# Kernel optimization log

Hardware: AMD Instinct MI355X
Metric: run time of the kernel (lower is better)

## Reference

```python
import jax, jax.numpy as jnp
import numpy as np

N_VOX = 150000
GRID = 256
C_IN = 32
C_OUT = 64
EPS = 1e-5


def _build_neighbor_idx(n=N_VOX, g=GRID, seed=0):
    # Build a submanifold-conv rulebook: for each of 27 kernel offsets and each
    # output voxel, the index of the input voxel at that offset, or -1 if absent.
    rng = np.random.default_rng(seed)
    lin = rng.choice(g ** 3, size=n, replace=False).astype(np.int64)
    coords = np.stack(np.unravel_index(lin, (g, g, g)), axis=1)  # [N,3]
    order = np.argsort(lin)
    sorted_keys = lin[order]
    offs = np.array([[dx, dy, dz] for dx in (-1, 0, 1) for dy in (-1, 0, 1) for dz in (-1, 0, 1)], dtype=np.int64)  # [27,3]
    nbr = np.full((27, n), -1, dtype=np.int32)
    for k in range(27):
        nc = coords + offs[k]  # neighbor coords [N,3]
        valid = np.all((nc >= 0) & (nc < g), axis=1)
        nkey = (nc[:, 0] * g + nc[:, 1]) * g + nc[:, 2]
        pos = np.searchsorted(sorted_keys, nkey)
        pos_c = np.clip(pos, 0, n - 1)
        found = valid & (sorted_keys[pos_c] == nkey)
        nbr[k] = np.where(found, order[pos_c].astype(np.int32), -1)
    return jnp.asarray(nbr)


def setup_inputs() -> dict:
    key = jax.random.key(0)
    k1, k2, k3, k4 = jax.random.split(key, 4)
    features = jax.random.normal(k1, (N_VOX, C_IN), dtype=jnp.float32)
    weight = jax.random.normal(k2, (27, C_IN, C_OUT), dtype=jnp.float32) * 0.05
    gamma = jax.random.uniform(k3, (C_OUT,), dtype=jnp.float32, minval=0.5, maxval=1.5)
    beta = jax.random.normal(k4, (C_OUT,), dtype=jnp.float32) * 0.1
    neighbor_idx = _build_neighbor_idx()
    return {"features": features, "weight": weight, "gamma": gamma, "beta": beta, "neighbor_idx": neighbor_idx}


def reference(features, weight, gamma, beta, neighbor_idx):
    # --- SubMConv3d via rulebook gather -> GEMM -> (implicit) scatter ---
    safe_idx = jnp.maximum(neighbor_idx, 0)            # [K,N]
    gathered = features[safe_idx]                      # [K,N,Cin]
    mask = (neighbor_idx >= 0)[..., None]              # [K,N,1]
    gathered = jnp.where(mask, gathered, jnp.zeros((), features.dtype))
    out = jnp.einsum('knc,kcd->nd', gathered, weight)  # [N,Cout]
    # --- BatchNorm1d (training-mode batch stats, biased var) + ReLU ---
    mean = jnp.mean(out, axis=0)
    var = jnp.mean(jnp.square(out - mean), axis=0)
    normed = (out - mean) * jax.lax.rsqrt(var + EPS)
    return jax.nn.relu(normed * gamma + beta)
```

## Files before the change

kernel.cpp:

```cpp
#include <hip/hip_runtime.h>

#define NV    150000
#define CIN   32
#define COUT  64
#define EPSF  1e-5f
#define NCOPY 16

#define NTHR   256
#define NTILES (NV / 16)
#define NBLK1  ((NTILES + 3) / 4)

#define CH8    (NV * COUT / 8)
#define NBLK2  1172
#define STRIDE2 (NBLK2 * NTHR)

#define WS_WFRAG  0
#define WS_GSTATS 110592
#define WS_OUTBF  118784

typedef short  bf16x8 __attribute__((ext_vector_type(8)));
typedef float  f32x4  __attribute__((ext_vector_type(4)));

union u4bf { uint4 u; bf16x8 h; };

__device__ __forceinline__ unsigned pack_bf2(float a, float b) {
    union { float f; unsigned u; } ca, cb;
    ca.f = a; cb.f = b;
    const unsigned lo = (ca.u + 0x7FFFu + ((ca.u >> 16) & 1u)) >> 16;
    const unsigned hi = (cb.u + 0x7FFFu + ((cb.u >> 16) & 1u)) & 0xFFFF0000u;
    return lo | hi;
}

__device__ __forceinline__ unsigned short bf16r(float a) {
    union { float f; unsigned u; } c; c.f = a;
    return (unsigned short)((c.u + 0x7FFFu + ((c.u >> 16) & 1u)) >> 16);
}

__device__ __forceinline__ u4bf pack_row(float4 f0, float4 f1) {
    u4bf r;
    r.u.x = pack_bf2(f0.x, f0.y);
    r.u.y = pack_bf2(f0.z, f0.w);
    r.u.z = pack_bf2(f1.x, f1.y);
    r.u.w = pack_bf2(f1.z, f1.w);
    return r;
}

__global__ __launch_bounds__(NTHR) void k_prep(
    const float* __restrict__ weight,
    char*        __restrict__ ws)
{
    const int b = blockIdx.x;
    if (b < 27) {
        const int k    = b;
        const int bb   = threadIdx.x >> 6;
        const int lane = threadIdx.x & 63;
        const int quad = lane >> 4;
        const int lm   = lane & 15;
        const float* wsrc = weight + (long)k * CIN * COUT + (quad * 8) * COUT + bb * 16 + lm;
        float f[8];
#pragma unroll
        for (int j = 0; j < 8; ++j) f[j] = wsrc[j * COUT];
        uint4 o;
        o.x = pack_bf2(f[0], f[1]);
        o.y = pack_bf2(f[2], f[3]);
        o.z = pack_bf2(f[4], f[5]);
        o.w = pack_bf2(f[6], f[7]);
        ((uint4*)(ws + WS_WFRAG))[(k * 4 + bb) * 64 + lane] = o;
    } else {
        float* gs = (float*)(ws + WS_GSTATS);
#pragma unroll
        for (int i = 0; i < 8; ++i) gs[threadIdx.x + i * NTHR] = 0.f;
    }
}

__global__ __launch_bounds__(NTHR) void k_conv(
    const float* __restrict__ feat,
    char*        __restrict__ ws,
    const int*   __restrict__ nbr,
    float*       __restrict__ gstats)
{
    const uint4* wf = (const uint4*)(ws + WS_WFRAG);
    unsigned short* ob = (unsigned short*)(ws + WS_OUTBF);

    const int tid  = threadIdx.x;
    const int lane = tid & 63;
    const int quad = lane >> 4;
    const int lm   = lane & 15;
    const int wid  = blockIdx.x * 4 + (tid >> 6);

    f32x4 ssum = {0.f, 0.f, 0.f, 0.f};
    f32x4 qsum = {0.f, 0.f, 0.f, 0.f};
    f32x4 acc[4] = {{0.f,0.f,0.f,0.f},{0.f,0.f,0.f,0.f},{0.f,0.f,0.f,0.f},{0.f,0.f,0.f,0.f}};

    const bool have_tile = (wid < NTILES);
    const int v0 = have_tile ? wid * 16 : 0;

    if (have_tile) {
        int sidx[7];
#pragma unroll
        for (int it = 0; it < 7; ++it) {
            const int item = lane + it * 64;
            int idx = -1;
            if (item < 416) {
                const int kp = item >> 4;
                const int k  = kp + (kp >= 13);
                idx = nbr[(long)k * NV + v0 + (item & 15)];
            }
            sidx[it] = idx;
        }

        {
            const float4* fp = (const float4*)(feat + (long)(v0 + lm) * CIN + quad * 8);
            const u4bf a0 = pack_row(fp[0], fp[1]);
#pragma unroll
            for (int b = 0; b < 4; ++b) {
                u4bf w; w.u = wf[(13 * 4 + b) * 64 + lane];
                acc[b] = __builtin_amdgcn_mfma_f32_16x16x32_bf16(a0.h, w.h, acc[b], 0, 0, 0);
            }
        }

        unsigned int kmask = 0u;
#pragma unroll
        for (int it = 0; it < 7; ++it) {
            const unsigned long long m = __ballot(sidx[it] >= 0);
            kmask |= ((m & 0xFFFFull)         ? 1u : 0u) << (it * 4 + 0);
            kmask |= (((m >> 16) & 0xFFFFull) ? 1u : 0u) << (it * 4 + 1);
            kmask |= (((m >> 32) & 0xFFFFull) ? 1u : 0u) << (it * 4 + 2);
            kmask |= ((m >> 48)               ? 1u : 0u) << (it * 4 + 3);
        }

        while (kmask) {
            const int kpA = __ffs(kmask) - 1;
            kmask &= kmask - 1u;
            int kpB = -1;
            if (kmask) { kpB = __ffs(kmask) - 1; kmask &= kmask - 1u; }
            const int kA = kpA + (kpA >= 13);
            const int kB = (kpB >= 0) ? (kpB + (kpB >= 13)) : kA;

            int rawA, rawB;
            switch (kpA >> 2) {
                case 0: rawA = sidx[0]; break; case 1: rawA = sidx[1]; break;
                case 2: rawA = sidx[2]; break; case 3: rawA = sidx[3]; break;
                case 4: rawA = sidx[4]; break; case 5: rawA = sidx[5]; break;
                default: rawA = sidx[6]; break;
            }
            const int kpB2 = (kpB >= 0) ? kpB : kpA;
            switch (kpB2 >> 2) {
                case 0: rawB = sidx[0]; break; case 1: rawB = sidx[1]; break;
                case 2: rawB = sidx[2]; break; case 3: rawB = sidx[3]; break;
                case 4: rawB = sidx[4]; break; case 5: rawB = sidx[5]; break;
                default: rawB = sidx[6]; break;
            }
            const int idxA = __shfl(rawA, ((kpA & 3) << 4) | lm);
            int idxB = __shfl(rawB, ((kpB2 & 3) << 4) | lm);
            if (kpB < 0) idxB = -1;

            const float4* fpA = (const float4*)(feat + (long)(idxA < 0 ? 0 : idxA) * CIN + quad * 8);
            const float4* fpB = (const float4*)(feat + (long)(idxB < 0 ? 0 : idxB) * CIN + quad * 8);
            u4bf aA = pack_row(fpA[0], fpA[1]);
            u4bf aB = pack_row(fpB[0], fpB[1]);
            if (idxA < 0) aA.u = make_uint4(0u, 0u, 0u, 0u);
            if (idxB < 0) aB.u = make_uint4(0u, 0u, 0u, 0u);

#pragma unroll
            for (int b = 0; b < 4; ++b) {
                u4bf wA, wB;
                wA.u = wf[(kA * 4 + b) * 64 + lane];
                wB.u = wf[(kB * 4 + b) * 64 + lane];
                acc[b] = __builtin_amdgcn_mfma_f32_16x16x32_bf16(aA.h, wA.h, acc[b], 0, 0, 0);
                acc[b] = __builtin_amdgcn_mfma_f32_16x16x32_bf16(aB.h, wB.h, acc[b], 0, 0, 0);
            }
        }

#pragma unroll
        for (int b = 0; b < 4; ++b) {
            const float r0 = acc[b][0], r1 = acc[b][1], r2 = acc[b][2], r3 = acc[b][3];
            ob[(long)(v0 + quad * 4 + 0) * COUT + b * 16 + lm] = bf16r(r0);
            ob[(long)(v0 + quad * 4 + 1) * COUT + b * 16 + lm] = bf16r(r1);
            ob[(long)(v0 + quad * 4 + 2) * COUT + b * 16 + lm] = bf16r(r2);
            ob[(long)(v0 + quad * 4 + 3) * COUT + b * 16 + lm] = bf16r(r3);
            ssum[b] += r0 + r1 + r2 + r3;
            qsum[b] += r0 * r0 + r1 * r1 + r2 * r2 + r3 * r3;
        }
    }

#pragma unroll
    for (int off = 16; off < 64; off <<= 1) {
#pragma unroll
        for (int b = 0; b < 4; ++b) {
            ssum[b] += __shfl_xor(ssum[b], off);
            qsum[b] += __shfl_xor(qsum[b], off);
        }
    }

    __shared__ float ls[4][128];
    const int wv = tid >> 6;
    if (quad == 0) {
#pragma unroll
        for (int b = 0; b < 4; ++b) {
            ls[wv][b * 16 + lm]      = ssum[b];
            ls[wv][64 + b * 16 + lm] = qsum[b];
        }
    }
    __syncthreads();
    if (tid < 128) {
        const float v = ls[0][tid] + ls[1][tid] + ls[2][tid] + ls[3][tid];
        atomicAdd(gstats + (blockIdx.x & (NCOPY - 1)) * 128 + tid, v);
    }
}

__global__ __launch_bounds__(NTHR) void k_norm(
    const char*  __restrict__ ws_ro,
    float*       __restrict__ out,
    const float* __restrict__ gstats,
    const float* __restrict__ gamma,
    const float* __restrict__ beta)
{
    __shared__ float sscale[COUT];
    __shared__ float sshift[COUT];
    const int tid = threadIdx.x;
    if (tid < COUT) {
        float s = 0.f, q = 0.f;
#pragma unroll
        for (int cp = 0; cp < NCOPY; ++cp) {
            s += gstats[cp * 128 + tid];
            q += gstats[cp * 128 + 64 + tid];
        }
        const float inv_n = 1.f / (float)NV;
        const float mean = s * inv_n;
        float var = q * inv_n - mean * mean;
        var = fmaxf(var, 0.f);
        const float rstd = rsqrtf(var + EPSF);
        const float sc = gamma[tid] * rstd;
        sscale[tid] = sc;
        sshift[tid] = beta[tid] - mean * sc;
    }
    __syncthreads();

    const int  base = blockIdx.x * NTHR + tid;
    const int  g8   = (base & 7) * 8;
    const float4 SC0 = make_float4(sscale[g8],   sscale[g8+1], sscale[g8+2], sscale[g8+3]);
    const float4 SC1 = make_float4(sscale[g8+4], sscale[g8+5], sscale[g8+6], sscale[g8+7]);
    const float4 SH0 = make_float4(sshift[g8],   sshift[g8+1], sshift[g8+2], sshift[g8+3]);
    const float4 SH1 = make_float4(sshift[g8+4], sshift[g8+5], sshift[g8+6], sshift[g8+7]);

    const uint4* ib = (const uint4*)(ws_ro + WS_OUTBF);
    float4* o4 = (float4*)out;

#pragma unroll
    for (int n = 0; n < 4; ++n) {
        const int c = base + n * STRIDE2;
        if (n == 3 && c >= CH8) break;
        const uint4 u = ib[c];
        union { unsigned u; float f; } t;
        float4 v0, v1;
        t.u = u.x << 16;          v0.x = t.f;
        t.u = u.x & 0xFFFF0000u;  v0.y = t.f;
        t.u = u.y << 16;          v0.z = t.f;
        t.u = u.y & 0xFFFF0000u;  v0.w = t.f;
        t.u = u.z << 16;          v1.x = t.f;
        t.u = u.z & 0xFFFF0000u;  v1.y = t.f;
        t.u = u.w << 16;          v1.z = t.f;
        t.u = u.w & 0xFFFF0000u;  v1.w = t.f;

        v0.x = fmaxf(v0.x * SC0.x + SH0.x, 0.f);
        v0.y = fmaxf(v0.y * SC0.y + SH0.y, 0.f);
        v0.z = fmaxf(v0.z * SC0.z + SH0.z, 0.f);
        v0.w = fmaxf(v0.w * SC0.w + SH0.w, 0.f);
        v1.x = fmaxf(v1.x * SC1.x + SH1.x, 0.f);
        v1.y = fmaxf(v1.y * SC1.y + SH1.y, 0.f);
        v1.z = fmaxf(v1.z * SC1.z + SH1.z, 0.f);
        v1.w = fmaxf(v1.w * SC1.w + SH1.w, 0.f);

        o4[(long)c * 2]     = v0;
        o4[(long)c * 2 + 1] = v1;
    }
}

extern "C" void kernel_launch(void* const* d_in, const int* in_sizes, int n_in,
                              void* d_out, int out_size, void* d_ws, size_t ws_size,
                              hipStream_t stream) {
    const float* feat   = (const float*)d_in[0];
    const float* weight = (const float*)d_in[1];
    const float* gamma  = (const float*)d_in[2];
    const float* beta   = (const float*)d_in[3];
    const int*   nbr    = (const int*)d_in[4];
    float* out = (float*)d_out;

    char*  ws     = (char*)d_ws;
    float* gstats = (float*)(ws + WS_GSTATS);

    k_prep<<<28, NTHR, 0, stream>>>(weight, ws);
    k_conv<<<NBLK1, NTHR, 0, stream>>>(feat, ws, nbr, gstats);
    k_norm<<<NBLK2, NTHR, 0, stream>>>(ws, out, gstats, gamma, beta);
}
```

Baseline: 114.7 us.

## Fuse conv and batchnorm into persistent kernel with grid barrier

Merges the conv and normalize kernels into one persistent kernel of 512 blocks, where each wave handles 5 tiles and keeps their accumulators in registers. A software grid barrier on an atomic counter waits for the global statistics before scale and shift are applied straight from registers. This removes the bf16 intermediate write and re-read and one kernel launch, and prefetches the next tile's neighbor indices. In exchange it needs all 512 blocks co-resident (launch bounds set to 2 blocks per CU), uses far more registers per wave, and its output stores are narrow scalar writes.

```diff
diff --git a/kernel.cpp b/kernel.cpp
--- a/kernel.cpp
+++ b/kernel.cpp
@@ -8,15 +8,13 @@
 
 #define NTHR   256
 #define NTILES (NV / 16)
-#define NBLK1  ((NTILES + 3) / 4)
-
-#define CH8    (NV * COUT / 8)
-#define NBLK2  1172
-#define STRIDE2 (NBLK2 * NTHR)
+#define NBLKF  512
+#define WAVES_TOT (NBLKF * 4)
+#define TPW    5
 
 #define WS_WFRAG  0
 #define WS_GSTATS 110592
-#define WS_OUTBF  118784
+#define WS_BAR    (WS_GSTATS + NCOPY * 128 * 4)
 
 typedef short  bf16x8 __attribute__((ext_vector_type(8)));
 typedef float  f32x4  __attribute__((ext_vector_type(4)));
@@ -29,11 +27,6 @@
     const unsigned lo = (ca.u + 0x7FFFu + ((ca.u >> 16) & 1u)) >> 16;
     const unsigned hi = (cb.u + 0x7FFFu + ((cb.u >> 16) & 1u)) & 0xFFFF0000u;
     return lo | hi;
-}
-
-__device__ __forceinline__ unsigned short bf16r(float a) {
-    union { float f; unsigned u; } c; c.f = a;
-    return (unsigned short)((c.u + 0x7FFFu + ((c.u >> 16) & 1u)) >> 16);
 }
 
 __device__ __forceinline__ u4bf pack_row(float4 f0, float4 f1) {
@@ -69,18 +62,37 @@
     } else {
         float* gs = (float*)(ws + WS_GSTATS);
 #pragma unroll
-        for (int i = 0; i < 8; ++i) gs[threadIdx.x + i * NTHR] = 0.f;
-    }
-}
-
-__global__ __launch_bounds__(NTHR) void k_conv(
+        for (int i = 0; i < 9; ++i) gs[threadIdx.x + i * NTHR] = 0.f;
+    }
+}
+
+__device__ __forceinline__ void load_sidx(
+    const int* __restrict__ nbr, int v0, bool have, int lane, int sidx[7])
+{
+#pragma unroll
+    for (int it = 0; it < 7; ++it) {
+        const int item = lane + it * 64;
+        int idx = -1;
+        if (have && item < 416) {
+            const int kp = item >> 4;
+            const int k  = kp + (kp >= 13);
+            idx = nbr[(long)k * NV + v0 + (item & 15)];
+        }
+        sidx[it] = idx;
+    }
+}
+
+__global__ __launch_bounds__(NTHR, 2) void k_fused(
     const float* __restrict__ feat,
     char*        __restrict__ ws,
     const int*   __restrict__ nbr,
-    float*       __restrict__ gstats)
+    float*       __restrict__ gstats,
+    float*       __restrict__ out,
+    const float* __restrict__ gamma,
+    const float* __restrict__ beta)
 {
     const uint4* wf = (const uint4*)(ws + WS_WFRAG);
-    unsigned short* ob = (unsigned short*)(ws + WS_OUTBF);
+    unsigned* bar = (unsigned*)(ws + WS_BAR);
 
     const int tid  = threadIdx.x;
     const int lane = tid & 63;
@@ -90,97 +102,103 @@
 
     f32x4 ssum = {0.f, 0.f, 0.f, 0.f};
     f32x4 qsum = {0.f, 0.f, 0.f, 0.f};
-    f32x4 acc[4] = {{0.f,0.f,0.f,0.f},{0.f,0.f,0.f,0.f},{0.f,0.f,0.f,0.f},{0.f,0.f,0.f,0.f}};
-
-    const bool have_tile = (wid < NTILES);
-    const int v0 = have_tile ? wid * 16 : 0;
-
-    if (have_tile) {
-        int sidx[7];
-#pragma unroll
-        for (int it = 0; it < 7; ++it) {
-            const int item = lane + it * 64;
-            int idx = -1;
-            if (item < 416) {
-                const int kp = item >> 4;
-                const int k  = kp + (kp >= 13);
-                idx = nbr[(long)k * NV + v0 + (item & 15)];
-            }
-            sidx[it] = idx;
-        }
-
-        {
-            const float4* fp = (const float4*)(feat + (long)(v0 + lm) * CIN + quad * 8);
-            const u4bf a0 = pack_row(fp[0], fp[1]);
+    f32x4 acc[TPW][4];
+#pragma unroll
+    for (int t = 0; t < TPW; ++t)
+#pragma unroll
+        for (int b = 0; b < 4; ++b) acc[t][b] = (f32x4){0.f, 0.f, 0.f, 0.f};
+
+    int sidx[7];
+    load_sidx(nbr, wid * 16, wid < NTILES, lane, sidx);
+
+#pragma unroll
+    for (int t = 0; t < TPW; ++t) {
+        const int tile = wid + t * WAVES_TOT;
+        const bool have = (tile < NTILES);
+        const int v0 = tile * 16;
+
+        int snxt[7];
+        if (t + 1 < TPW) {
+            const int tn = wid + (t + 1) * WAVES_TOT;
+            load_sidx(nbr, tn * 16, tn < NTILES, lane, snxt);
+        }
+
+        if (have) {
+            {
+                const float4* fp = (const float4*)(feat + (long)(v0 + lm) * CIN + quad * 8);
+                const u4bf a0 = pack_row(fp[0], fp[1]);
+#pragma unroll
+                for (int b = 0; b < 4; ++b) {
+                    u4bf w; w.u = wf[(13 * 4 + b) * 64 + lane];
+                    acc[t][b] = __builtin_amdgcn_mfma_f32_16x16x32_bf16(a0.h, w.h, acc[t][b], 0, 0, 0);
+                }
+            }
+
+            unsigned int kmask = 0u;
+#pragma unroll
+            for (int it = 0; it < 7; ++it) {
+                const unsigned long long m = __ballot(sidx[it] >= 0);
+                kmask |= ((m & 0xFFFFull)         ? 1u : 0u) << (it * 4 + 0);
+                kmask |= (((m >> 16) & 0xFFFFull) ? 1u : 0u) << (it * 4 + 1);
+                kmask |= (((m >> 32) & 0xFFFFull) ? 1u : 0u) << (it * 4 + 2);
+                kmask |= ((m >> 48)               ? 1u : 0u) << (it * 4 + 3);
+            }
+
+            while (kmask) {
+                const int kpA = __ffs(kmask) - 1;
+                kmask &= kmask - 1u;
+                int kpB = -1;
+                if (kmask) { kpB = __ffs(kmask) - 1; kmask &= kmask - 1u; }
+                const int kA = kpA + (kpA >= 13);
+                const int kB = (kpB >= 0) ? (kpB + (kpB >= 13)) : kA;
+
+                int rawA, rawB;
+                switch (kpA >> 2) {
+                    case 0: rawA = sidx[0]; break; case 1: rawA = sidx[1]; break;
+                    case 2: rawA = sidx[2]; break; case 3: rawA = sidx[3]; break;
+                    case 4: rawA = sidx[4]; break; case 5: rawA = sidx[5]; break;
+                    default: rawA = sidx[6]; break;
+                }
+                const int kpB2 = (kpB >= 0) ? kpB : kpA;
+                switch (kpB2 >> 2) {
+                    case 0: rawB = sidx[0]; break; case 1: rawB = sidx[1]; break;
+                    case 2: rawB = sidx[2]; break; case 3: rawB = sidx[3]; break;
+                    case 4: rawB = sidx[4]; break; case 5: rawB = sidx[5]; break;
+                    default: rawB = sidx[6]; break;
+                }
+                const int idxA = __shfl(rawA, ((kpA & 3) << 4) | lm);
+                int idxB = __shfl(rawB, ((kpB2 & 3) << 4) | lm);
+                if (kpB < 0) idxB = -1;
+
+                const float4* fpA = (const float4*)(feat + (long)(idxA < 0 ? 0 : idxA) * CIN + quad * 8);
+                const float4* fpB = (const float4*)(feat + (long)(idxB < 0 ? 0 : idxB) * CIN + quad * 8);
+                u4bf aA = pack_row(fpA[0], fpA[1]);
+                u4bf aB = pack_row(fpB[0], fpB[1]);
+                if (idxA < 0) aA.u = make_uint4(0u, 0u, 0u, 0u);
+                if (idxB < 0) aB.u = make_uint4(0u, 0u, 0u, 0u);
+
+#pragma unroll
+                for (int b = 0; b < 4; ++b) {
+                    u4bf wA, wB;
+                    wA.u = wf[(kA * 4 + b) * 64 + lane];
+                    wB.u = wf[(kB * 4 + b) * 64 + lane];
+                    acc[t][b] = __builtin_amdgcn_mfma_f32_16x16x32_bf16(aA.h, wA.h, acc[t][b], 0, 0, 0);
+                    acc[t][b] = __builtin_amdgcn_mfma_f32_16x16x32_bf16(aB.h, wB.h, acc[t][b], 0, 0, 0);
+                }
+            }
+
 #pragma unroll
             for (int b = 0; b < 4; ++b) {
-                u4bf w; w.u = wf[(13 * 4 + b) * 64 + lane];
-                acc[b] = __builtin_amdgcn_mfma_f32_16x16x32_bf16(a0.h, w.h, acc[b], 0, 0, 0);
-            }
-        }
-
-        unsigned int kmask = 0u;
-#pragma unroll
-        for (int it = 0; it < 7; ++it) {
-            const unsigned long long m = __ballot(sidx[it] >= 0);
-            kmask |= ((m & 0xFFFFull)         ? 1u : 0u) << (it * 4 + 0);
-            kmask |= (((m >> 16) & 0xFFFFull) ? 1u : 0u) << (it * 4 + 1);
-            kmask |= (((m >> 32) & 0xFFFFull) ? 1u : 0u) << (it * 4 + 2);
-            kmask |= ((m >> 48)               ? 1u : 0u) << (it * 4 + 3);
-        }
-
-        while (kmask) {
-            const int kpA = __ffs(kmask) - 1;
-            kmask &= kmask - 1u;
-            int kpB = -1;
-            if (kmask) { kpB = __ffs(kmask) - 1; kmask &= kmask - 1u; }
-            const int kA = kpA + (kpA >= 13);
-            const int kB = (kpB >= 0) ? (kpB + (kpB >= 13)) : kA;
-
-            int rawA, rawB;
-            switch (kpA >> 2) {
-                case 0: rawA = sidx[0]; break; case 1: rawA = sidx[1]; break;
-                case 2: rawA = sidx[2]; break; case 3: rawA = sidx[3]; break;
-                case 4: rawA = sidx[4]; break; case 5: rawA = sidx[5]; break;
-                default: rawA = sidx[6]; break;
-            }
-            const int kpB2 = (kpB >= 0) ? kpB : kpA;
-            switch (kpB2 >> 2) {
-                case 0: rawB = sidx[0]; break; case 1: rawB = sidx[1]; break;
-                case 2: rawB = sidx[2]; break; case 3: rawB = sidx[3]; break;
-                case 4: rawB = sidx[4]; break; case 5: rawB = sidx[5]; break;
-                default: rawB = sidx[6]; break;
-            }
-            const int idxA = __shfl(rawA, ((kpA & 3) << 4) | lm);
-            int idxB = __shfl(rawB, ((kpB2 & 3) << 4) | lm);
-            if (kpB < 0) idxB = -1;
-
-            const float4* fpA = (const float4*)(feat + (long)(idxA < 0 ? 0 : idxA) * CIN + quad * 8);
-            const float4* fpB = (const float4*)(feat + (long)(idxB < 0 ? 0 : idxB) * CIN + quad * 8);
-            u4bf aA = pack_row(fpA[0], fpA[1]);
-            u4bf aB = pack_row(fpB[0], fpB[1]);
-            if (idxA < 0) aA.u = make_uint4(0u, 0u, 0u, 0u);
-            if (idxB < 0) aB.u = make_uint4(0u, 0u, 0u, 0u);
-
-#pragma unroll
-            for (int b = 0; b < 4; ++b) {
-                u4bf wA, wB;
-                wA.u = wf[(kA * 4 + b) * 64 + lane];
-                wB.u = wf[(kB * 4 + b) * 64 + lane];
-                acc[b] = __builtin_amdgcn_mfma_f32_16x16x32_bf16(aA.h, wA.h, acc[b], 0, 0, 0);
-                acc[b] = __builtin_amdgcn_mfma_f32_16x16x32_bf16(aB.h, wB.h, acc[b], 0, 0, 0);
-            }
-        }
-
-#pragma unroll
-        for (int b = 0; b < 4; ++b) {
-            const float r0 = acc[b][0], r1 = acc[b][1], r2 = acc[b][2], r3 = acc[b][3];
-            ob[(long)(v0 + quad * 4 + 0) * COUT + b * 16 + lm] = bf16r(r0);
-            ob[(long)(v0 + quad * 4 + 1) * COUT + b * 16 + lm] = bf16r(r1);
-            ob[(long)(v0 + quad * 4 + 2) * COUT + b * 16 + lm] = bf16r(r2);
-            ob[(long)(v0 + quad * 4 + 3) * COUT + b * 16 + lm] = bf16r(r3);
-            ssum[b] += r0 + r1 + r2 + r3;
-            qsum[b] += r0 * r0 + r1 * r1 + r2 * r2 + r3 * r3;
+                const float r0 = acc[t][b][0], r1 = acc[t][b][1];
+                const float r2 = acc[t][b][2], r3 = acc[t][b][3];
+                ssum[b] += r0 + r1 + r2 + r3;
+                qsum[b] += r0 * r0 + r1 * r1 + r2 * r2 + r3 * r3;
+            }
+        }
+
+        if (t + 1 < TPW) {
+#pragma unroll
+            for (int it = 0; it < 7; ++it) sidx[it] = snxt[it];
         }
     }
 
@@ -207,24 +225,25 @@
         const float v = ls[0][tid] + ls[1][tid] + ls[2][tid] + ls[3][tid];
         atomicAdd(gstats + (blockIdx.x & (NCOPY - 1)) * 128 + tid, v);
     }
-}
-
-__global__ __launch_bounds__(NTHR) void k_norm(
-    const char*  __restrict__ ws_ro,
-    float*       __restrict__ out,
-    const float* __restrict__ gstats,
-    const float* __restrict__ gamma,
-    const float* __restrict__ beta)
-{
+    __syncthreads();
+
+    if (tid == 0) {
+        __threadfence();
+        __hip_atomic_fetch_add(bar, 1u, __ATOMIC_ACQ_REL, __HIP_MEMORY_SCOPE_AGENT);
+        while (__hip_atomic_load(bar, __ATOMIC_ACQUIRE, __HIP_MEMORY_SCOPE_AGENT) < (unsigned)NBLKF) {
+            __builtin_amdgcn_s_sleep(8);
+        }
+    }
+    __syncthreads();
+
     __shared__ float sscale[COUT];
     __shared__ float sshift[COUT];
-    const int tid = threadIdx.x;
     if (tid < COUT) {
         float s = 0.f, q = 0.f;
 #pragma unroll
         for (int cp = 0; cp < NCOPY; ++cp) {
-            s += gstats[cp * 128 + tid];
-            q += gstats[cp * 128 + 64 + tid];
+            s += __hip_atomic_load(gstats + cp * 128 + tid, __ATOMIC_RELAXED, __HIP_MEMORY_SCOPE_AGENT);
+            q += __hip_atomic_load(gstats + cp * 128 + 64 + tid, __ATOMIC_RELAXED, __HIP_MEMORY_SCOPE_AGENT);
         }
         const float inv_n = 1.f / (float)NV;
         const float mean = s * inv_n;
@@ -237,43 +256,26 @@
     }
     __syncthreads();
 
-    const int  base = blockIdx.x * NTHR + tid;
-    const int  g8   = (base & 7) * 8;
-    const float4 SC0 = make_float4(sscale[g8],   sscale[g8+1], sscale[g8+2], sscale[g8+3]);
-    const float4 SC1 = make_float4(sscale[g8+4], sscale[g8+5], sscale[g8+6], sscale[g8+7]);
-    const float4 SH0 = make_float4(sshift[g8],   sshift[g8+1], sshift[g8+2], sshift[g8+3]);
-    const float4 SH1 = make_float4(sshift[g8+4], sshift[g8+5], sshift[g8+6], sshift[g8+7]);
-
-    const uint4* ib = (const uint4*)(ws_ro + WS_OUTBF);
-    float4* o4 = (float4*)out;
-
-#pragma unroll
-    for (int n = 0; n < 4; ++n) {
-        const int c = base + n * STRIDE2;
-        if (n == 3 && c >= CH8) break;
-        const uint4 u = ib[c];
-        union { unsigned u; float f; } t;
-        float4 v0, v1;
-        t.u = u.x << 16;          v0.x = t.f;
-        t.u = u.x & 0xFFFF0000u;  v0.y = t.f;
-        t.u = u.y << 16;          v0.z = t.f;
-        t.u = u.y & 0xFFFF0000u;  v0.w = t.f;
-        t.u = u.z << 16;          v1.x = t.f;
-        t.u = u.z & 0xFFFF0000u;  v1.y = t.f;
-        t.u = u.w << 16;          v1.z = t.f;
-        t.u = u.w & 0xFFFF0000u;  v1.w = t.f;
-
-        v0.x = fmaxf(v0.x * SC0.x + SH0.x, 0.f);
-        v0.y = fmaxf(v0.y * SC0.y + SH0.y, 0.f);
-        v0.z = fmaxf(v0.z * SC0.z + SH0.z, 0.f);
-        v0.w = fmaxf(v0.w * SC0.w + SH0.w, 0.f);
-        v1.x = fmaxf(v1.x * SC1.x + SH1.x, 0.f);
-        v1.y = fmaxf(v1.y * SC1.y + SH1.y, 0.f);
-        v1.z = fmaxf(v1.z * SC1.z + SH1.z, 0.f);
-        v1.w = fmaxf(v1.w * SC1.w + SH1.w, 0.f);
-
-        o4[(long)c * 2]     = v0;
-        o4[(long)c * 2 + 1] = v1;
+    float scv[4], shv[4];
+#pragma unroll
+    for (int b = 0; b < 4; ++b) {
+        scv[b] = sscale[b * 16 + lm];
+        shv[b] = sshift[b * 16 + lm];
+    }
+
+#pragma unroll
+    for (int t = 0; t < TPW; ++t) {
+        const int tile = wid + t * WAVES_TOT;
+        if (tile >= NTILES) continue;
+        const int v0 = tile * 16;
+#pragma unroll
+        for (int b = 0; b < 4; ++b) {
+#pragma unroll
+            for (int r = 0; r < 4; ++r) {
+                out[(long)(v0 + quad * 4 + r) * COUT + b * 16 + lm] =
+                    fmaxf(acc[t][b][r] * scv[b] + shv[b], 0.f);
+            }
+        }
     }
 }
 
@@ -291,6 +293,5 @@
     float* gstats = (float*)(ws + WS_GSTATS);
 
     k_prep<<<28, NTHR, 0, stream>>>(weight, ws);
-    k_conv<<<NBLK1, NTHR, 0, stream>>>(feat, ws, nbr, gstats);
-    k_norm<<<NBLK2, NTHR, 0, stream>>>(ws, out, gstats, gamma, beta);
-}
+    k_fused<<<NBLKF, NTHR, 0, stream>>>(feat, ws, nbr, gstats, out, gamma, beta);
+}
```

New measurement: 210.6 us. +83.6%, slower.

## Split conv into dense center-offset MFMA pass and sparse atomic scatter pass

Applied to the files above, without the earlier changes.

Replaces the per-tile rulebook conv with two kernels. A dense kernel computes only the center offset with bf16 MFMA and writes an fp32 intermediate. A sparse kernel then walks each of the other 26 offsets, does an fp32 dot product for each valid neighbor, and scatters it with atomicAdd. Batch statistics are updated incrementally from the value returned by each atomic, so the squared-sum terms telescope to the final total. The aim is to avoid per-tile index gathering and MFMA work on the very sparse neighbor sets, at the cost of an extra launch, atomic traffic, and an fp32 intermediate buffer twice the size of the previous bf16 one.

```diff
diff --git a/kernel.cpp b/kernel.cpp
--- a/kernel.cpp
+++ b/kernel.cpp
@@ -5,18 +5,19 @@
 #define COUT  64
 #define EPSF  1e-5f
 #define NCOPY 16
-
-#define NTHR   256
-#define NTILES (NV / 16)
-#define NBLK1  ((NTILES + 3) / 4)
-
-#define CH8    (NV * COUT / 8)
-#define NBLK2  1172
-#define STRIDE2 (NBLK2 * NTHR)
-
-#define WS_WFRAG  0
-#define WS_GSTATS 110592
-#define WS_OUTBF  118784
+#define NTHR  256
+
+#define NTILES 9375
+#define NBLKD  2344
+#define VBLK   586
+#define NBLK3  1172
+#define STRIDE3 (NBLK3 * NTHR)
+#define CH4    (NV * COUT / 4)
+
+#define WS_WT     0
+#define WS_W13    221184
+#define WS_GSTATS 225280
+#define WS_OUTF   233472
 
 typedef short  bf16x8 __attribute__((ext_vector_type(8)));
 typedef float  f32x4  __attribute__((ext_vector_type(4)));
@@ -29,11 +30,6 @@
     const unsigned lo = (ca.u + 0x7FFFu + ((ca.u >> 16) & 1u)) >> 16;
     const unsigned hi = (cb.u + 0x7FFFu + ((cb.u >> 16) & 1u)) & 0xFFFF0000u;
     return lo | hi;
-}
-
-__device__ __forceinline__ unsigned short bf16r(float a) {
-    union { float f; unsigned u; } c; c.f = a;
-    return (unsigned short)((c.u + 0x7FFFu + ((c.u >> 16) & 1u)) >> 16);
 }
 
 __device__ __forceinline__ u4bf pack_row(float4 f0, float4 f1) {
@@ -51,12 +47,22 @@
 {
     const int b = blockIdx.x;
     if (b < 27) {
-        const int k    = b;
+        const int k = b;
+        float* wt = (float*)(ws + WS_WT) + (long)k * COUT * CIN;
+        const float* wsrc = weight + (long)k * CIN * COUT;
+#pragma unroll
+        for (int e = 0; e < 8; ++e) {
+            const int idx = threadIdx.x + e * NTHR;
+            const int ci  = idx >> 6;
+            const int co  = idx & 63;
+            wt[co * CIN + ci] = wsrc[ci * COUT + co];
+        }
+    } else if (b == 27) {
         const int bb   = threadIdx.x >> 6;
         const int lane = threadIdx.x & 63;
         const int quad = lane >> 4;
         const int lm   = lane & 15;
-        const float* wsrc = weight + (long)k * CIN * COUT + (quad * 8) * COUT + bb * 16 + lm;
+        const float* wsrc = weight + (long)13 * CIN * COUT + (quad * 8) * COUT + bb * 16 + lm;
         float f[8];
 #pragma unroll
         for (int j = 0; j < 8; ++j) f[j] = wsrc[j * COUT];
@@ -65,7 +71,7 @@
         o.y = pack_bf2(f[2], f[3]);
         o.z = pack_bf2(f[4], f[5]);
         o.w = pack_bf2(f[6], f[7]);
-        ((uint4*)(ws + WS_WFRAG))[(k * 4 + bb) * 64 + lane] = o;
+        ((uint4*)(ws + WS_W13))[bb * 64 + lane] = o;
     } else {
         float* gs = (float*)(ws + WS_GSTATS);
 #pragma unroll
@@ -73,112 +79,41 @@
     }
 }
 
-__global__ __launch_bounds__(NTHR) void k_conv(
+__global__ __launch_bounds__(NTHR) void k_dense(
     const float* __restrict__ feat,
     char*        __restrict__ ws,
-    const int*   __restrict__ nbr,
     float*       __restrict__ gstats)
 {
-    const uint4* wf = (const uint4*)(ws + WS_WFRAG);
-    unsigned short* ob = (unsigned short*)(ws + WS_OUTBF);
+    const uint4* wf = (const uint4*)(ws + WS_W13);
+    float* outf = (float*)(ws + WS_OUTF);
 
     const int tid  = threadIdx.x;
     const int lane = tid & 63;
     const int quad = lane >> 4;
     const int lm   = lane & 15;
     const int wid  = blockIdx.x * 4 + (tid >> 6);
+    const bool have = (wid < NTILES);
+    const int v0 = have ? wid * 16 : 0;
 
     f32x4 ssum = {0.f, 0.f, 0.f, 0.f};
     f32x4 qsum = {0.f, 0.f, 0.f, 0.f};
     f32x4 acc[4] = {{0.f,0.f,0.f,0.f},{0.f,0.f,0.f,0.f},{0.f,0.f,0.f,0.f},{0.f,0.f,0.f,0.f}};
 
-    const bool have_tile = (wid < NTILES);
-    const int v0 = have_tile ? wid * 16 : 0;
-
-    if (have_tile) {
-        int sidx[7];
-#pragma unroll
-        for (int it = 0; it < 7; ++it) {
-            const int item = lane + it * 64;
-            int idx = -1;
-            if (item < 416) {
-                const int kp = item >> 4;
-                const int k  = kp + (kp >= 13);
-                idx = nbr[(long)k * NV + v0 + (item & 15)];
-            }
-            sidx[it] = idx;
-        }
-
-        {
-            const float4* fp = (const float4*)(feat + (long)(v0 + lm) * CIN + quad * 8);
-            const u4bf a0 = pack_row(fp[0], fp[1]);
-#pragma unroll
-            for (int b = 0; b < 4; ++b) {
-                u4bf w; w.u = wf[(13 * 4 + b) * 64 + lane];
-                acc[b] = __builtin_amdgcn_mfma_f32_16x16x32_bf16(a0.h, w.h, acc[b], 0, 0, 0);
-            }
-        }
-
-        unsigned int kmask = 0u;
-#pragma unroll
-        for (int it = 0; it < 7; ++it) {
-            const unsigned long long m = __ballot(sidx[it] >= 0);
-            kmask |= ((m & 0xFFFFull)         ? 1u : 0u) << (it * 4 + 0);
-            kmask |= (((m >> 16) & 0xFFFFull) ? 1u : 0u) << (it * 4 + 1);
-            kmask |= (((m >> 32) & 0xFFFFull) ? 1u : 0u) << (it * 4 + 2);
-            kmask |= ((m >> 48)               ? 1u : 0u) << (it * 4 + 3);
-        }
-
-        while (kmask) {
-            const int kpA = __ffs(kmask) - 1;
-            kmask &= kmask - 1u;
-            int kpB = -1;
-            if (kmask) { kpB = __ffs(kmask) - 1; kmask &= kmask - 1u; }
-            const int kA = kpA + (kpA >= 13);
-            const int kB = (kpB >= 0) ? (kpB + (kpB >= 13)) : kA;
-
-            int rawA, rawB;
-            switch (kpA >> 2) {
-                case 0: rawA = sidx[0]; break; case 1: rawA = sidx[1]; break;
-                case 2: rawA = sidx[2]; break; case 3: rawA = sidx[3]; break;
-                case 4: rawA = sidx[4]; break; case 5: rawA = sidx[5]; break;
-                default: rawA = sidx[6]; break;
-            }
-            const int kpB2 = (kpB >= 0) ? kpB : kpA;
-            switch (kpB2 >> 2) {
-                case 0: rawB = sidx[0]; break; case 1: rawB = sidx[1]; break;
-                case 2: rawB = sidx[2]; break; case 3: rawB = sidx[3]; break;
-                case 4: rawB = sidx[4]; break; case 5: rawB = sidx[5]; break;
-                default: rawB = sidx[6]; break;
-            }
-            const int idxA = __shfl(rawA, ((kpA & 3) << 4) | lm);
-            int idxB = __shfl(rawB, ((kpB2 & 3) << 4) | lm);
-            if (kpB < 0) idxB = -1;
-
-            const float4* fpA = (const float4*)(feat + (long)(idxA < 0 ? 0 : idxA) * CIN + quad * 8);
-            const float4* fpB = (const float4*)(feat + (long)(idxB < 0 ? 0 : idxB) * CIN + quad * 8);
-            u4bf aA = pack_row(fpA[0], fpA[1]);
-            u4bf aB = pack_row(fpB[0], fpB[1]);
-            if (idxA < 0) aA.u = make_uint4(0u, 0u, 0u, 0u);
-            if (idxB < 0) aB.u = make_uint4(0u, 0u, 0u, 0u);
-
-#pragma unroll
-            for (int b = 0; b < 4; ++b) {
-                u4bf wA, wB;
-                wA.u = wf[(kA * 4 + b) * 64 + lane];
-                wB.u = wf[(kB * 4 + b) * 64 + lane];
-                acc[b] = __builtin_amdgcn_mfma_f32_16x16x32_bf16(aA.h, wA.h, acc[b], 0, 0, 0);
-                acc[b] = __builtin_amdgcn_mfma_f32_16x16x32_bf16(aB.h, wB.h, acc[b], 0, 0, 0);
-            }
-        }
-
+    if (have) {
+        const float4* fp = (const float4*)(feat + (long)(v0 + lm) * CIN + quad * 8);
+        const u4bf a0 = pack_row(fp[0], fp[1]);
+#pragma unroll
+        for (int b = 0; b < 4; ++b) {
+            u4bf w; w.u = wf[b * 64 + lane];
+            acc[b] = __builtin_amdgcn_mfma_f32_16x16x32_bf16(a0.h, w.h, acc[b], 0, 0, 0);
+        }
 #pragma unroll
         for (int b = 0; b < 4; ++b) {
             const float r0 = acc[b][0], r1 = acc[b][1], r2 = acc[b][2], r3 = acc[b][3];
-            ob[(long)(v0 + quad * 4 + 0) * COUT + b * 16 + lm] = bf16r(r0);
-            ob[(long)(v0 + quad * 4 + 1) * COUT + b * 16 + lm] = bf16r(r1);
-            ob[(long)(v0 + quad * 4 + 2) * COUT + b * 16 + lm] = bf16r(r2);
-            ob[(long)(v0 + quad * 4 + 3) * COUT + b * 16 + lm] = bf16r(r3);
+            outf[(long)(v0 + quad * 4 + 0) * COUT + b * 16 + lm] = r0;
+            outf[(long)(v0 + quad * 4 + 1) * COUT + b * 16 + lm] = r1;
+            outf[(long)(v0 + quad * 4 + 2) * COUT + b * 16 + lm] = r2;
+            outf[(long)(v0 + quad * 4 + 3) * COUT + b * 16 + lm] = r3;
             ssum[b] += r0 + r1 + r2 + r3;
             qsum[b] += r0 * r0 + r1 * r1 + r2 * r2 + r3 * r3;
         }
@@ -206,6 +141,58 @@
     if (tid < 128) {
         const float v = ls[0][tid] + ls[1][tid] + ls[2][tid] + ls[3][tid];
         atomicAdd(gstats + (blockIdx.x & (NCOPY - 1)) * 128 + tid, v);
+    }
+}
+
+__global__ __launch_bounds__(NTHR) void k_sparse(
+    const float* __restrict__ feat,
+    char*        __restrict__ ws,
+    const int*   __restrict__ nbr,
+    float*       __restrict__ gstats)
+{
+    const int kp = blockIdx.y;
+    const int k  = kp + (kp >= 13);
+    const int v  = blockIdx.x * NTHR + (int)threadIdx.x;
+    const int lane = threadIdx.x & 63;
+
+    float* outf = (float*)(ws + WS_OUTF);
+    const float* wt = (const float*)(ws + WS_WT) + (long)k * COUT * CIN;
+
+    int idx = -1;
+    if (v < NV) idx = nbr[(long)k * NV + v];
+
+    unsigned long long mask = __ballot(idx >= 0);
+    const bool any = (mask != 0ull);
+    float sd = 0.f, qd = 0.f;
+
+    const float4* wl = (const float4*)(wt + lane * CIN);
+
+    while (mask) {
+        const int l = __ffsll(mask) - 1;
+        mask &= mask - 1ull;
+        const int j = __shfl(idx, l);
+        const int i = __shfl(v, l);
+
+        const float4* fj = (const float4*)(feat + (long)j * CIN);
+        float a = 0.f;
+#pragma unroll
+        for (int e = 0; e < 8; ++e) {
+            const float4 f = fj[e];
+            const float4 w = wl[e];
+            a = fmaf(f.x, w.x, a);
+            a = fmaf(f.y, w.y, a);
+            a = fmaf(f.z, w.z, a);
+            a = fmaf(f.w, w.w, a);
+        }
+        const float old = atomicAdd(outf + (long)i * COUT + lane, a);
+        sd += a;
+        qd += a * (a + 2.f * old);
+    }
+
+    if (any) {
+        float* gs = gstats + ((blockIdx.x + blockIdx.y) & (NCOPY - 1)) * 128;
+        atomicAdd(gs + lane, sd);
+        atomicAdd(gs + 64 + lane, qd);
     }
 }
 
@@ -237,43 +224,24 @@
     }
     __syncthreads();
 
-    const int  base = blockIdx.x * NTHR + tid;
-    const int  g8   = (base & 7) * 8;
-    const float4 SC0 = make_float4(sscale[g8],   sscale[g8+1], sscale[g8+2], sscale[g8+3]);
-    const float4 SC1 = make_float4(sscale[g8+4], sscale[g8+5], sscale[g8+6], sscale[g8+7]);
-    const float4 SH0 = make_float4(sshift[g8],   sshift[g8+1], sshift[g8+2], sshift[g8+3]);
-    const float4 SH1 = make_float4(sshift[g8+4], sshift[g8+5], sshift[g8+6], sshift[g8+7]);
-
-    const uint4* ib = (const uint4*)(ws_ro + WS_OUTBF);
+    const int base = blockIdx.x * NTHR + tid;
+    const int g    = (base & 15) * 4;
+    const float4 SC = make_float4(sscale[g], sscale[g+1], sscale[g+2], sscale[g+3]);
+    const float4 SH = make_float4(sshift[g], sshift[g+1], sshift[g+2], sshift[g+3]);
+
+    const float4* ib = (const float4*)(ws_ro + WS_OUTF);
     float4* o4 = (float4*)out;
 
 #pragma unroll
-    for (int n = 0; n < 4; ++n) {
-        const int c = base + n * STRIDE2;
-        if (n == 3 && c >= CH8) break;
-        const uint4 u = ib[c];
-        union { unsigned u; float f; } t;
-        float4 v0, v1;
-        t.u = u.x << 16;          v0.x = t.f;
-        t.u = u.x & 0xFFFF0000u;  v0.y = t.f;
-        t.u = u.y << 16;          v0.z = t.f;
-        t.u = u.y & 0xFFFF0000u;  v0.w = t.f;
-        t.u = u.z << 16;          v1.x = t.f;
-        t.u = u.z & 0xFFFF0000u;  v1.y = t.f;
-        t.u = u.w << 16;          v1.z = t.f;
-        t.u = u.w & 0xFFFF0000u;  v1.w = t.f;
-
-        v0.x = fmaxf(v0.x * SC0.x + SH0.x, 0.f);
-        v0.y = fmaxf(v0.y * SC0.y + SH0.y, 0.f);
-        v0.z = fmaxf(v0.z * SC0.z + SH0.z, 0.f);
-        v0.w = fmaxf(v0.w * SC0.w + SH0.w, 0.f);
-        v1.x = fmaxf(v1.x * SC1.x + SH1.x, 0.f);
-        v1.y = fmaxf(v1.y * SC1.y + SH1.y, 0.f);
-        v1.z = fmaxf(v1.z * SC1.z + SH1.z, 0.f);
-        v1.w = fmaxf(v1.w * SC1.w + SH1.w, 0.f);
-
-        o4[(long)c * 2]     = v0;
-        o4[(long)c * 2 + 1] = v1;
+    for (int n = 0; n < 8; ++n) {
+        const int c = base + n * STRIDE3;
+        if (c >= CH4) break;
+        float4 v = ib[c];
+        v.x = fmaxf(v.x * SC.x + SH.x, 0.f);
+        v.y = fmaxf(v.y * SC.y + SH.y, 0.f);
+        v.z = fmaxf(v.z * SC.z + SH.z, 0.f);
+        v.w = fmaxf(v.w * SC.w + SH.w, 0.f);
+        o4[c] = v;
     }
 }
 
@@ -290,7 +258,8 @@
     char*  ws     = (char*)d_ws;
     float* gstats = (float*)(ws + WS_GSTATS);
 
-    k_prep<<<28, NTHR, 0, stream>>>(weight, ws);
-    k_conv<<<NBLK1, NTHR, 0, stream>>>(feat, ws, nbr, gstats);
-    k_norm<<<NBLK2, NTHR, 0, stream>>>(ws, out, gstats, gamma, beta);
-}
+    k_prep<<<29, NTHR, 0, stream>>>(weight, ws);
+    k_dense<<<NBLKD, NTHR, 0, stream>>>(feat, ws, gstats);
+    k_sparse<<<dim3(VBLK, 26), NTHR, 0, stream>>>(feat, ws, nbr, gstats);
+    k_norm<<<NBLK3, NTHR, 0, stream>>>(ws, out, gstats, gamma, beta);
+}
```

Result: slower. 162.5 us (+41.7%).

## Replace per-offset MFMA tiles with per-neighbor wave-wide dot products

Applied to the files above, without the earlier changes.

The conv kernel no longer runs bf16 MFMA over 16-row tiles for each kernel offset that has any valid neighbor. It now loops over individual valid neighbor entries found by ballot. For each one, the whole wave loads that input row, computes all 64 output channels as fp32 FMAs against bf16 weights stored transposed per offset, and shuffles the results into the MFMA accumulator layout. The goal is to stop spending MFMA work and 16-row gathers on tiles that are mostly empty in a very sparse grid. The cost is a serial per-neighbor loop with extra shuffles and divergent switch updates, plus a new transposed weight layout built in the prep kernel.

```diff
diff --git a/kernel.cpp b/kernel.cpp
--- a/kernel.cpp
+++ b/kernel.cpp
@@ -5,8 +5,8 @@
 #define COUT  64
 #define EPSF  1e-5f
 #define NCOPY 16
-
-#define NTHR   256
+#define NTHR  256
+
 #define NTILES (NV / 16)
 #define NBLK1  ((NTILES + 3) / 4)
 
@@ -14,9 +14,10 @@
 #define NBLK2  1172
 #define STRIDE2 (NBLK2 * NTHR)
 
-#define WS_WFRAG  0
-#define WS_GSTATS 110592
-#define WS_OUTBF  118784
+#define WS_W13    0
+#define WS_WTB    4096
+#define WS_GSTATS 114688
+#define WS_OUTBF  122880
 
 typedef short  bf16x8 __attribute__((ext_vector_type(8)));
 typedef float  f32x4  __attribute__((ext_vector_type(4)));
@@ -45,18 +46,41 @@
     return r;
 }
 
+__device__ __forceinline__ float dot8(float4 fa, float4 fb, uint4 w, float c) {
+    union { unsigned u; float f; } t;
+    t.u = w.x << 16;          c = fmaf(fa.x, t.f, c);
+    t.u = w.x & 0xFFFF0000u;  c = fmaf(fa.y, t.f, c);
+    t.u = w.y << 16;          c = fmaf(fa.z, t.f, c);
+    t.u = w.y & 0xFFFF0000u;  c = fmaf(fa.w, t.f, c);
+    t.u = w.z << 16;          c = fmaf(fb.x, t.f, c);
+    t.u = w.z & 0xFFFF0000u;  c = fmaf(fb.y, t.f, c);
+    t.u = w.w << 16;          c = fmaf(fb.z, t.f, c);
+    t.u = w.w & 0xFFFF0000u;  c = fmaf(fb.w, t.f, c);
+    return c;
+}
+
 __global__ __launch_bounds__(NTHR) void k_prep(
     const float* __restrict__ weight,
     char*        __restrict__ ws)
 {
     const int b = blockIdx.x;
     if (b < 27) {
-        const int k    = b;
+        const int k = b;
+        const float* wsrc = weight + (long)k * CIN * COUT;
+        unsigned* dst = (unsigned*)(ws + WS_WTB) + k * 1024;
+#pragma unroll
+        for (int e = 0; e < 4; ++e) {
+            const int w  = threadIdx.x * 4 + e;
+            const int co = w >> 4;
+            const int ci = (w & 15) * 2;
+            dst[w] = pack_bf2(wsrc[ci * COUT + co], wsrc[(ci + 1) * COUT + co]);
+        }
+    } else if (b == 27) {
         const int bb   = threadIdx.x >> 6;
         const int lane = threadIdx.x & 63;
         const int quad = lane >> 4;
         const int lm   = lane & 15;
-        const float* wsrc = weight + (long)k * CIN * COUT + (quad * 8) * COUT + bb * 16 + lm;
+        const float* wsrc = weight + (long)13 * CIN * COUT + (quad * 8) * COUT + bb * 16 + lm;
         float f[8];
 #pragma unroll
         for (int j = 0; j < 8; ++j) f[j] = wsrc[j * COUT];
@@ -65,7 +89,7 @@
         o.y = pack_bf2(f[2], f[3]);
         o.z = pack_bf2(f[4], f[5]);
         o.w = pack_bf2(f[6], f[7]);
-        ((uint4*)(ws + WS_WFRAG))[(k * 4 + bb) * 64 + lane] = o;
+        ((uint4*)(ws + WS_W13))[bb * 64 + lane] = o;
     } else {
         float* gs = (float*)(ws + WS_GSTATS);
 #pragma unroll
@@ -79,7 +103,8 @@
     const int*   __restrict__ nbr,
     float*       __restrict__ gstats)
 {
-    const uint4* wf = (const uint4*)(ws + WS_WFRAG);
+    const uint4* wf  = (const uint4*)(ws + WS_W13);
+    const uint4* wtb = (const uint4*)(ws + WS_WTB);
     unsigned short* ob = (unsigned short*)(ws + WS_OUTBF);
 
     const int tid  = threadIdx.x;
@@ -87,91 +112,76 @@
     const int quad = lane >> 4;
     const int lm   = lane & 15;
     const int wid  = blockIdx.x * 4 + (tid >> 6);
+    const bool have = (wid < NTILES);
+    const int v0 = have ? wid * 16 : 0;
 
     f32x4 ssum = {0.f, 0.f, 0.f, 0.f};
     f32x4 qsum = {0.f, 0.f, 0.f, 0.f};
     f32x4 acc[4] = {{0.f,0.f,0.f,0.f},{0.f,0.f,0.f,0.f},{0.f,0.f,0.f,0.f},{0.f,0.f,0.f,0.f}};
 
-    const bool have_tile = (wid < NTILES);
-    const int v0 = have_tile ? wid * 16 : 0;
-
-    if (have_tile) {
-        int sidx[7];
-#pragma unroll
-        for (int it = 0; it < 7; ++it) {
-            const int item = lane + it * 64;
-            int idx = -1;
-            if (item < 416) {
-                const int kp = item >> 4;
-                const int k  = kp + (kp >= 13);
-                idx = nbr[(long)k * NV + v0 + (item & 15)];
+    int sidx[7];
+#pragma unroll
+    for (int it = 0; it < 7; ++it) {
+        const int item = lane + it * 64;
+        int idx = -1;
+        if (have && item < 416) {
+            const int kp = item >> 4;
+            const int k  = kp + (kp >= 13);
+            idx = nbr[(long)k * NV + v0 + (item & 15)];
+        }
+        sidx[it] = idx;
+    }
+
+    if (have) {
+        const float4* fp = (const float4*)(feat + (long)(v0 + lm) * CIN + quad * 8);
+        const u4bf a0 = pack_row(fp[0], fp[1]);
+#pragma unroll
+        for (int b = 0; b < 4; ++b) {
+            u4bf w; w.u = wf[b * 64 + lane];
+            acc[b] = __builtin_amdgcn_mfma_f32_16x16x32_bf16(a0.h, w.h, acc[b], 0, 0, 0);
+        }
+    }
+
+#pragma unroll
+    for (int it = 0; it < 7; ++it) {
+        unsigned long long m = __ballot(sidx[it] >= 0);
+        while (m) {
+            const int l = __ffsll(m) - 1;
+            m &= m - 1ull;
+            const int item = it * 64 + l;
+            const int kp   = item >> 4;
+            const int k    = kp + (kp >= 13);
+            const int slot = item & 15;
+            const int j    = __shfl(sidx[it], l);
+
+            const float4* fj = (const float4*)(feat + (long)j * CIN);
+            float4 f0 = fj[0], f1 = fj[1], f2 = fj[2], f3 = fj[3];
+            float4 f4 = fj[4], f5 = fj[5], f6 = fj[6], f7 = fj[7];
+
+            const uint4* wr = wtb + ((k * 64 + lane) << 2);
+            const uint4 wA = wr[0], wB = wr[1], wC = wr[2], wD = wr[3];
+
+            float c = 0.f;
+            c = dot8(f0, f1, wA, c);
+            c = dot8(f2, f3, wB, c);
+            c = dot8(f4, f5, wC, c);
+            c = dot8(f6, f7, wD, c);
+
+            const float vb0 = __shfl(c, 0 * 16 + lm);
+            const float vb1 = __shfl(c, 1 * 16 + lm);
+            const float vb2 = __shfl(c, 2 * 16 + lm);
+            const float vb3 = __shfl(c, 3 * 16 + lm);
+            const int sq = slot >> 2;
+            switch (slot & 3) {
+                case 0: if (quad == sq) { acc[0][0]+=vb0; acc[1][0]+=vb1; acc[2][0]+=vb2; acc[3][0]+=vb3; } break;
+                case 1: if (quad == sq) { acc[0][1]+=vb0; acc[1][1]+=vb1; acc[2][1]+=vb2; acc[3][1]+=vb3; } break;
+                case 2: if (quad == sq) { acc[0][2]+=vb0; acc[1][2]+=vb1; acc[2][2]+=vb2; acc[3][2]+=vb3; } break;
+                default: if (quad == sq) { acc[0][3]+=vb0; acc[1][3]+=vb1; acc[2][3]+=vb2; acc[3][3]+=vb3; } break;
             }
-            sidx[it] = idx;
-        }
-
-        {
-            const float4* fp = (const float4*)(feat + (long)(v0 + lm) * CIN + quad * 8);
-            const u4bf a0 = pack_row(fp[0], fp[1]);
-#pragma unroll
-            for (int b = 0; b < 4; ++b) {
-                u4bf w; w.u = wf[(13 * 4 + b) * 64 + lane];
-                acc[b] = __builtin_amdgcn_mfma_f32_16x16x32_bf16(a0.h, w.h, acc[b], 0, 0, 0);
-            }
-        }
-
-        unsigned int kmask = 0u;
-#pragma unroll
-        for (int it = 0; it < 7; ++it) {
-            const unsigned long long m = __ballot(sidx[it] >= 0);
-            kmask |= ((m & 0xFFFFull)         ? 1u : 0u) << (it * 4 + 0);
-            kmask |= (((m >> 16) & 0xFFFFull) ? 1u : 0u) << (it * 4 + 1);
-            kmask |= (((m >> 32) & 0xFFFFull) ? 1u : 0u) << (it * 4 + 2);
-            kmask |= ((m >> 48)               ? 1u : 0u) << (it * 4 + 3);
-        }
-
-        while (kmask) {
-            const int kpA = __ffs(kmask) - 1;
-            kmask &= kmask - 1u;
-            int kpB = -1;
-            if (kmask) { kpB = __ffs(kmask) - 1; kmask &= kmask - 1u; }
-            const int kA = kpA + (kpA >= 13);
-            const int kB = (kpB >= 0) ? (kpB + (kpB >= 13)) : kA;
-
-            int rawA, rawB;
-            switch (kpA >> 2) {
-                case 0: rawA = sidx[0]; break; case 1: rawA = sidx[1]; break;
-                case 2: rawA = sidx[2]; break; case 3: rawA = sidx[3]; break;
-                case 4: rawA = sidx[4]; break; case 5: rawA = sidx[5]; break;
-                default: rawA = sidx[6]; break;
-            }
-            const int kpB2 = (kpB >= 0) ? kpB : kpA;
-            switch (kpB2 >> 2) {
-                case 0: rawB = sidx[0]; break; case 1: rawB = sidx[1]; break;
-                case 2: rawB = sidx[2]; break; case 3: rawB = sidx[3]; break;
-                case 4: rawB = sidx[4]; break; case 5: rawB = sidx[5]; break;
-                default: rawB = sidx[6]; break;
-            }
-            const int idxA = __shfl(rawA, ((kpA & 3) << 4) | lm);
-            int idxB = __shfl(rawB, ((kpB2 & 3) << 4) | lm);
-            if (kpB < 0) idxB = -1;
-
-            const float4* fpA = (const float4*)(feat + (long)(idxA < 0 ? 0 : idxA) * CIN + quad * 8);
-            const float4* fpB = (const float4*)(feat + (long)(idxB < 0 ? 0 : idxB) * CIN + quad * 8);
-            u4bf aA = pack_row(fpA[0], fpA[1]);
-            u4bf aB = pack_row(fpB[0], fpB[1]);
-            if (idxA < 0) aA.u = make_uint4(0u, 0u, 0u, 0u);
-            if (idxB < 0) aB.u = make_uint4(0u, 0u, 0u, 0u);
-
-#pragma unroll
-            for (int b = 0; b < 4; ++b) {
-                u4bf wA, wB;
-                wA.u = wf[(kA * 4 + b) * 64 + lane];
-                wB.u = wf[(kB * 4 + b) * 64 + lane];
-                acc[b] = __builtin_amdgcn_mfma_f32_16x16x32_bf16(aA.h, wA.h, acc[b], 0, 0, 0);
-                acc[b] = __builtin_amdgcn_mfma_f32_16x16x32_bf16(aB.h, wB.h, acc[b], 0, 0, 0);
-            }
-        }
-
+        }
+    }
+
+    if (have) {
 #pragma unroll
         for (int b = 0; b < 4; ++b) {
             const float r0 = acc[b][0], r1 = acc[b][1], r2 = acc[b][2], r3 = acc[b][3];
@@ -290,7 +300,7 @@
     char*  ws     = (char*)d_ws;
     float* gstats = (float*)(ws + WS_GSTATS);
 
-    k_prep<<<28, NTHR, 0, stream>>>(weight, ws);
+    k_prep<<<29, NTHR, 0, stream>>>(weight, ws);
     k_conv<<<NBLK1, NTHR, 0, stream>>>(feat, ws, nbr, gstats);
     k_norm<<<NBLK2, NTHR, 0, stream>>>(ws, out, gstats, gamma, beta);
 }
```

Result: slower. 124.6 us (+8.6%).
